# Performance work log

Measured on AMD Instinct MI355X. Metric: run time of the kernel, lower is better.

## Reference

```python
import jax, jax.numpy as jnp
import numpy as np

B, S, D = 8, 1024, 2048          # batch, seq_len, model dim (q_features == kv_features)
H, HD = 16, 128                   # num_heads, head_dim; H*HD == hidden == 2048


def setup_inputs() -> dict:
    key = jax.random.key(0)
    ks = jax.random.split(key, 6)
    fan_in = 1.0 / np.sqrt(D)     # variance_scaling(1.0, 'fan_in') style init scale
    return {
        "inputs_q": jax.random.normal(ks[0], (B, S, D), jnp.float32),
        "inputs_kv": jax.random.normal(ks[1], (B, S, D), jnp.float32),
        "Wq": jax.random.normal(ks[2], (D, H * HD), jnp.float32) * fan_in,
        "Wk": jax.random.normal(ks[3], (D, H * HD), jnp.float32) * fan_in,
        "Wv": jax.random.normal(ks[4], (D, H * HD), jnp.float32) * fan_in,
        "Wo": jax.random.normal(ks[5], (H * HD, D), jnp.float32) * (1.0 / np.sqrt(H * HD)),
    }


def reference(inputs_q, inputs_kv, Wq, Wk, Wv, Wo):
    b, sq, _ = inputs_q.shape
    skv = inputs_kv.shape[1]
    # QKV projections (DenseGeneral, no bias), reshape to heads
    # scale_attn_logits=True -> query scaled by 1/sqrt(head_dim)
    q = (inputs_q @ Wq).reshape(b, sq, H, HD) * (1.0 / np.sqrt(HD))
    k = (inputs_kv @ Wk).reshape(b, skv, H, HD)
    v = (inputs_kv @ Wv).reshape(b, skv, H, HD)
    # dot-product attention core: [b, h, q, k] scores -> softmax -> context
    scores = jnp.einsum('bqhd,bkhd->bhqk', q, k)
    attn = jax.nn.softmax(scores, axis=-1)
    ctx = jnp.einsum('bhqk,bkhd->bqhd', attn, v).reshape(b, sq, H * HD)
    # output projection back to q_features
    return ctx @ Wo
```

## Files before the change

kernel.cpp:

```cpp
#include <hip/hip_runtime.h>
#include <cstdint>
#include <cstddef>

#define B_  8
#define S_  1024
#define D_  2048
#define H_  16
#define HD_ 128

typedef __bf16 bf16x8 __attribute__((ext_vector_type(8)));
typedef float  f32x4  __attribute__((ext_vector_type(4)));

__device__ __forceinline__ unsigned short f2b(float f) {
    unsigned int u = __float_as_uint(f);
    unsigned int r = (u + 0x7fffu + ((u >> 16) & 1u)) >> 16;
    return (unsigned short)r;
}

__device__ __forceinline__ void gl2lds16(const void* g, void* l) {
    __builtin_amdgcn_global_load_lds(
        (const __attribute__((address_space(1))) void*)g,
        (__attribute__((address_space(3))) void*)l, 16, 0, 0);
}

__global__ void cvt_f32_bf16(const float* __restrict__ src,
                             unsigned short* __restrict__ dst, int n4) {
    int i = blockIdx.x * blockDim.x + threadIdx.x;
    if (i >= n4) return;
    float4 v = ((const float4*)src)[i];
    ushort4 o;
    o.x = f2b(v.x); o.y = f2b(v.y); o.z = f2b(v.z); o.w = f2b(v.w);
    ((ushort4*)dst)[i] = o;
}

__global__ void wtrans(const float* __restrict__ W, unsigned short* __restrict__ Wt) {
    __shared__ float tile[32][33];
    int bx = blockIdx.x, by = blockIdx.y;
    int tx = threadIdx.x, ty = threadIdx.y;
#pragma unroll
    for (int i = 0; i < 4; i++)
        tile[ty + i * 8][tx] = W[(size_t)(by * 32 + ty + i * 8) * D_ + bx * 32 + tx];
    __syncthreads();
#pragma unroll
    for (int i = 0; i < 4; i++)
        Wt[(size_t)(bx * 32 + ty + i * 8) * D_ + by * 32 + tx] = f2b(tile[tx][ty + i * 8]);
}

__global__ void vtrans(const unsigned short* __restrict__ V, unsigned short* __restrict__ Vt) {
    __shared__ unsigned short tile[32][33];
    int bh = blockIdx.z;
    int b = bh >> 4, h = bh & 15;
    int tx = threadIdx.x, ty = threadIdx.y;
    int s0 = blockIdx.x * 32, hd0 = blockIdx.y * 32;
#pragma unroll
    for (int i = 0; i < 4; i++)
        tile[ty + i * 8][tx] = V[(size_t)(b * S_ + s0 + ty + i * 8) * D_ + h * HD_ + hd0 + tx];
    __syncthreads();
#pragma unroll
    for (int i = 0; i < 4; i++)
        Vt[((size_t)bh * HD_ + hd0 + ty + i * 8) * S_ + s0 + tx] = tile[tx][ty + i * 8];
}

template <bool OUTF>
__global__ void gemm_bt(const unsigned short* __restrict__ A,
                        const unsigned short* __restrict__ Bt,
                        unsigned short* __restrict__ outB,
                        float* __restrict__ outF,
                        int M, int N, int K, float scale) {
    __shared__ unsigned short sA[128 * 64];
    __shared__ unsigned short sB[128 * 64];
    const int tid = threadIdx.x;
    const int w = tid >> 6, lane = tid & 63;
    const int l15 = lane & 15, lhi = lane >> 4;
    const int mBase = blockIdx.y * 128, nBase = blockIdx.x * 128;
    const int wm = (w >> 1) * 64, wn = (w & 1) * 64;

    int xoff[2];
#pragma unroll
    for (int ks = 0; ks < 2; ks++)
        xoff[ks] = (((ks * 4 + lhi) ^ (l15 & 7)) * 8);

    f32x4 acc[4][4] = {};

    for (int kb = 0; kb < K; kb += 64) {
        __syncthreads();
#pragma unroll
        for (int p = 0; p < 4; p++) {
            int c = p * 256 + tid;
            int row = c >> 3, pc = c & 7;
            int j = pc ^ (row & 7);
            gl2lds16(A  + (size_t)(mBase + row) * K + kb + j * 8, sA + c * 8);
            gl2lds16(Bt + (size_t)(nBase + row) * K + kb + j * 8, sB + c * 8);
        }
        __syncthreads();

#pragma unroll
        for (int ks = 0; ks < 2; ks++) {
            bf16x8 aF[4], bF[4];
#pragma unroll
            for (int i = 0; i < 4; i++)
                aF[i] = *(const bf16x8*)(sA + (wm + i * 16 + l15) * 64 + xoff[ks]);
#pragma unroll
            for (int j = 0; j < 4; j++)
                bF[j] = *(const bf16x8*)(sB + (wn + j * 16 + l15) * 64 + xoff[ks]);
#pragma unroll
            for (int i = 0; i < 4; i++)
#pragma unroll
                for (int j = 0; j < 4; j++)
                    acc[i][j] = __builtin_amdgcn_mfma_f32_16x16x32_bf16(aF[i], bF[j], acc[i][j], 0, 0, 0);
        }
    }

#pragma unroll
    for (int i = 0; i < 4; i++) {
#pragma unroll
        for (int j = 0; j < 4; j++) {
#pragma unroll
            for (int r = 0; r < 4; r++) {
                int row = mBase + wm + i * 16 + lhi * 4 + r;
                int col = nBase + wn + j * 16 + l15;
                float v = acc[i][j][r] * scale;
                if (OUTF) outF[(size_t)row * N + col] = v;
                else      outB[(size_t)row * N + col] = f2b(v);
            }
        }
    }
}

#define PSTR 72
__global__ void __launch_bounds__(256, 2)
attn(const unsigned short* __restrict__ Q,
     const unsigned short* __restrict__ Kb,
     const unsigned short* __restrict__ Vt,
     unsigned short* __restrict__ ctx) {
    __shared__ unsigned short sK[64 * 128];
    __shared__ unsigned short sV[128 * 64];
    __shared__ unsigned short sP[4 * 32 * PSTR];
    const int tid = threadIdx.x;
    const int w = tid >> 6, lane = tid & 63;
    const int l15 = lane & 15, lhi = lane >> 4;
    const int qt = blockIdx.x, h = blockIdx.y, b = blockIdx.z;
    const unsigned short* Qp = Q  + (size_t)b * S_ * D_ + h * HD_;
    const unsigned short* Kp = Kb + (size_t)b * S_ * D_ + h * HD_;
    const unsigned short* Vp = Vt + (size_t)(b * H_ + h) * HD_ * S_;
    const int q0 = qt * 128 + w * 32;

    int xoff[2];
#pragma unroll
    for (int ks = 0; ks < 2; ks++)
        xoff[ks] = (((ks * 4 + lhi) ^ (l15 & 7)) * 8);

    bf16x8 qF[2][4];
#pragma unroll
    for (int i = 0; i < 2; i++)
#pragma unroll
        for (int kk = 0; kk < 4; kk++)
            qF[i][kk] = *(const bf16x8*)(Qp + (size_t)(q0 + i * 16 + l15) * D_ + kk * 32 + lhi * 8);

    f32x4 o4[2][8] = {};
    float lrun[2][4] = {};
    unsigned short* sPw = sP + w * 32 * PSTR;

    for (int kt = 0; kt < S_ / 64; kt++) {
        __syncthreads();
#pragma unroll
        for (int p = 0; p < 4; p++) {
            int c = p * 256 + tid;
            {
                int row = c >> 4, pc = c & 15;
                int j = pc ^ (row & 7);
                gl2lds16(Kp + (size_t)(kt * 64 + row) * D_ + j * 8, sK + c * 8);
            }
            {
                int row = c >> 3, pc = c & 7;
                int j = pc ^ (row & 7);
                gl2lds16(Vp + (size_t)row * S_ + kt * 64 + j * 8, sV + c * 8);
            }
        }
        __syncthreads();

        f32x4 s4[2][4] = {};
#pragma unroll
        for (int j = 0; j < 4; j++) {
#pragma unroll
            for (int kk = 0; kk < 4; kk++) {
                bf16x8 bF = *(const bf16x8*)(sK + (j * 16 + l15) * 128 + ((kk * 4 + lhi) ^ (l15 & 7)) * 8);
#pragma unroll
                for (int i = 0; i < 2; i++)
                    s4[i][j] = __builtin_amdgcn_mfma_f32_16x16x32_bf16(qF[i][kk], bF, s4[i][j], 0, 0, 0);
            }
        }

#pragma unroll
        for (int i = 0; i < 2; i++) {
#pragma unroll
            for (int r = 0; r < 4; r++) {
                int prow = i * 16 + lhi * 4 + r;
                float ps = 0.f;
#pragma unroll
                for (int j = 0; j < 4; j++) {
                    float pv = exp2f(s4[i][j][r]);
                    ps += pv;
                    sPw[prow * PSTR + j * 16 + l15] = f2b(pv);
                }
                lrun[i][r] += ps;
            }
        }

#pragma unroll
        for (int k2 = 0; k2 < 2; k2++) {
            bf16x8 pF[2];
#pragma unroll
            for (int i = 0; i < 2; i++)
                pF[i] = *(const bf16x8*)(sPw + (i * 16 + l15) * PSTR + k2 * 32 + lhi * 8);
#pragma unroll
            for (int nt = 0; nt < 8; nt++) {
                bf16x8 vF = *(const bf16x8*)(sV + (nt * 16 + l15) * 64 + xoff[k2]);
#pragma unroll
                for (int i = 0; i < 2; i++)
                    o4[i][nt] = __builtin_amdgcn_mfma_f32_16x16x32_bf16(pF[i], vF, o4[i][nt], 0, 0, 0);
            }
        }
    }

#pragma unroll
    for (int i = 0; i < 2; i++)
#pragma unroll
        for (int r = 0; r < 4; r++) {
            float s = lrun[i][r];
#pragma unroll
            for (int msk = 1; msk < 16; msk <<= 1) s += __shfl_xor(s, msk);
            lrun[i][r] = 1.0f / s;
        }
#pragma unroll
    for (int i = 0; i < 2; i++)
#pragma unroll
        for (int nt = 0; nt < 8; nt++)
#pragma unroll
            for (int r = 0; r < 4; r++) {
                size_t row = (size_t)b * S_ + q0 + i * 16 + lhi * 4 + r;
                ctx[row * D_ + h * HD_ + nt * 16 + l15] = f2b(o4[i][nt][r] * lrun[i][r]);
            }
}

extern "C" void kernel_launch(void* const* d_in, const int* in_sizes, int n_in,
                              void* d_out, int out_size, void* d_ws, size_t ws_size,
                              hipStream_t stream) {
    const float* Xq  = (const float*)d_in[0];
    const float* Xkv = (const float*)d_in[1];
    const float* Wq  = (const float*)d_in[2];
    const float* Wk  = (const float*)d_in[3];
    const float* Wv  = (const float*)d_in[4];
    const float* Wo  = (const float*)d_in[5];
    float* out = (float*)d_out;

    char* ws = (char*)d_ws;
    const size_t XSZ = (size_t)B_ * S_ * D_ * 2;
    const size_t WSZ = (size_t)D_ * D_ * 2;
    unsigned short* XqB  = (unsigned short*)(ws);
    unsigned short* XkvB = (unsigned short*)(ws + XSZ);
    unsigned short* WqT  = (unsigned short*)(ws + 2 * XSZ);
    unsigned short* WkT  = (unsigned short*)(ws + 2 * XSZ + WSZ);
    unsigned short* WvT  = (unsigned short*)(ws + 2 * XSZ + 2 * WSZ);
    unsigned short* WoT  = (unsigned short*)(ws + 2 * XSZ + 3 * WSZ);
    unsigned short* Qb   = (unsigned short*)(ws + 3 * XSZ);
    unsigned short* Kb   = (unsigned short*)(ws + 4 * XSZ);
    unsigned short* Vb   = (unsigned short*)(ws + 5 * XSZ);
    unsigned short* VtB  = XkvB;
    unsigned short* ctxB = XqB;

    const int n4 = B_ * S_ * D_ / 4;
    cvt_f32_bf16<<<n4 / 256, 256, 0, stream>>>(Xq,  XqB,  n4);
    cvt_f32_bf16<<<n4 / 256, 256, 0, stream>>>(Xkv, XkvB, n4);

    dim3 tb(32, 8);
    wtrans<<<dim3(64, 64), tb, 0, stream>>>(Wq, WqT);
    wtrans<<<dim3(64, 64), tb, 0, stream>>>(Wk, WkT);
    wtrans<<<dim3(64, 64), tb, 0, stream>>>(Wv, WvT);
    wtrans<<<dim3(64, 64), tb, 0, stream>>>(Wo, WoT);

    const float qscale = 1.44269504088896f / 11.313708498984761f;
    dim3 gg(D_ / 128, B_ * S_ / 128);
    gemm_bt<false><<<gg, 256, 0, stream>>>(XqB,  WqT, Qb, nullptr, B_ * S_, D_, D_, qscale);
    gemm_bt<false><<<gg, 256, 0, stream>>>(XkvB, WkT, Kb, nullptr, B_ * S_, D_, D_, 1.0f);
    gemm_bt<false><<<gg, 256, 0, stream>>>(XkvB, WvT, Vb, nullptr, B_ * S_, D_, D_, 1.0f);

    vtrans<<<dim3(S_ / 32, HD_ / 32, B_ * H_), tb, 0, stream>>>(Vb, VtB);

    attn<<<dim3(S_ / 128, H_, B_), 256, 0, stream>>>(Qb, Kb, VtB, ctxB);

    gemm_bt<true><<<gg, 256, 0, stream>>>(ctxB, WoT, nullptr, out, B_ * S_, D_, D_, 1.0f);
}
```

Baseline: 629.7 us.

## Batch QKV projections into one launch and enlarge GEMM tile to 256x128

Replaces the generic 128x128 GEMM with a 256x128 tile kernel in which each wave computes 128x64 outputs, reusing each B fragment across eight A fragments. The three Q/K/V projections are merged into a single grid, with blockIdx.x choosing the region and its pointers, so three launches become one and the grid is larger and fuller. The output projection uses the same kernel. In exchange it needs more accumulator registers per thread (launch bounds 256,2) and more LDS per block, which may limit occupancy.

```diff
diff --git a/kernel.cpp b/kernel.cpp
--- a/kernel.cpp
+++ b/kernel.cpp
@@ -62,57 +62,71 @@
 }
 
 template <bool OUTF>
-__global__ void gemm_bt(const unsigned short* __restrict__ A,
-                        const unsigned short* __restrict__ Bt,
-                        unsigned short* __restrict__ outB,
-                        float* __restrict__ outF,
-                        int M, int N, int K, float scale) {
-    __shared__ unsigned short sA[128 * 64];
+__global__ void __launch_bounds__(256, 2)
+gemm_bt2(const unsigned short* __restrict__ A0, const unsigned short* __restrict__ A1,
+         const unsigned short* __restrict__ A2,
+         const unsigned short* __restrict__ B0, const unsigned short* __restrict__ B1,
+         const unsigned short* __restrict__ B2,
+         unsigned short* __restrict__ o0, unsigned short* __restrict__ o1,
+         unsigned short* __restrict__ o2, float* __restrict__ oF,
+         float s0, float s1, float s2) {
+    __shared__ unsigned short sA[256 * 64];
     __shared__ unsigned short sB[128 * 64];
     const int tid = threadIdx.x;
     const int w = tid >> 6, lane = tid & 63;
     const int l15 = lane & 15, lhi = lane >> 4;
-    const int mBase = blockIdx.y * 128, nBase = blockIdx.x * 128;
-    const int wm = (w >> 1) * 64, wn = (w & 1) * 64;
+    const int region = blockIdx.x >> 4;
+    const unsigned short* A  = region == 0 ? A0 : (region == 1 ? A1 : A2);
+    const unsigned short* Bt = region == 0 ? B0 : (region == 1 ? B1 : B2);
+    unsigned short* outB     = region == 0 ? o0 : (region == 1 ? o1 : o2);
+    const float scale        = region == 0 ? s0 : (region == 1 ? s1 : s2);
+    const int mBase = blockIdx.y * 256;
+    const int nBase = (blockIdx.x & 15) * 128;
+    const int wm = (w >> 1) * 128, wn = (w & 1) * 64;
 
     int xoff[2];
 #pragma unroll
     for (int ks = 0; ks < 2; ks++)
         xoff[ks] = (((ks * 4 + lhi) ^ (l15 & 7)) * 8);
 
-    f32x4 acc[4][4] = {};
-
-    for (int kb = 0; kb < K; kb += 64) {
+    f32x4 acc[8][4] = {};
+
+    for (int kb = 0; kb < D_; kb += 64) {
         __syncthreads();
+#pragma unroll
+        for (int p = 0; p < 8; p++) {
+            int c = p * 256 + tid;
+            int row = c >> 3, pc = c & 7;
+            int j = pc ^ (row & 7);
+            gl2lds16(A + (size_t)(mBase + row) * D_ + kb + j * 8, sA + c * 8);
+        }
 #pragma unroll
         for (int p = 0; p < 4; p++) {
             int c = p * 256 + tid;
             int row = c >> 3, pc = c & 7;
             int j = pc ^ (row & 7);
-            gl2lds16(A  + (size_t)(mBase + row) * K + kb + j * 8, sA + c * 8);
-            gl2lds16(Bt + (size_t)(nBase + row) * K + kb + j * 8, sB + c * 8);
+            gl2lds16(Bt + (size_t)(nBase + row) * D_ + kb + j * 8, sB + c * 8);
         }
         __syncthreads();
 
 #pragma unroll
         for (int ks = 0; ks < 2; ks++) {
-            bf16x8 aF[4], bF[4];
-#pragma unroll
-            for (int i = 0; i < 4; i++)
-                aF[i] = *(const bf16x8*)(sA + (wm + i * 16 + l15) * 64 + xoff[ks]);
+            bf16x8 bF[4];
 #pragma unroll
             for (int j = 0; j < 4; j++)
                 bF[j] = *(const bf16x8*)(sB + (wn + j * 16 + l15) * 64 + xoff[ks]);
 #pragma unroll
-            for (int i = 0; i < 4; i++)
+            for (int i = 0; i < 8; i++) {
+                bf16x8 aF = *(const bf16x8*)(sA + (wm + i * 16 + l15) * 64 + xoff[ks]);
 #pragma unroll
                 for (int j = 0; j < 4; j++)
-                    acc[i][j] = __builtin_amdgcn_mfma_f32_16x16x32_bf16(aF[i], bF[j], acc[i][j], 0, 0, 0);
+                    acc[i][j] = __builtin_amdgcn_mfma_f32_16x16x32_bf16(aF, bF[j], acc[i][j], 0, 0, 0);
+            }
         }
     }
 
 #pragma unroll
-    for (int i = 0; i < 4; i++) {
+    for (int i = 0; i < 8; i++) {
 #pragma unroll
         for (int j = 0; j < 4; j++) {
 #pragma unroll
@@ -120,8 +134,8 @@
                 int row = mBase + wm + i * 16 + lhi * 4 + r;
                 int col = nBase + wn + j * 16 + l15;
                 float v = acc[i][j][r] * scale;
-                if (OUTF) outF[(size_t)row * N + col] = v;
-                else      outB[(size_t)row * N + col] = f2b(v);
+                if (OUTF) oF[(size_t)row * D_ + col] = v;
+                else      outB[(size_t)row * D_ + col] = f2b(v);
             }
         }
     }
@@ -280,14 +294,14 @@
     wtrans<<<dim3(64, 64), tb, 0, stream>>>(Wo, WoT);
 
     const float qscale = 1.44269504088896f / 11.313708498984761f;
-    dim3 gg(D_ / 128, B_ * S_ / 128);
-    gemm_bt<false><<<gg, 256, 0, stream>>>(XqB,  WqT, Qb, nullptr, B_ * S_, D_, D_, qscale);
-    gemm_bt<false><<<gg, 256, 0, stream>>>(XkvB, WkT, Kb, nullptr, B_ * S_, D_, D_, 1.0f);
-    gemm_bt<false><<<gg, 256, 0, stream>>>(XkvB, WvT, Vb, nullptr, B_ * S_, D_, D_, 1.0f);
+
+    gemm_bt2<false><<<dim3(48, 32), 256, 0, stream>>>(
+        XqB, XkvB, XkvB, WqT, WkT, WvT, Qb, Kb, Vb, nullptr, qscale, 1.0f, 1.0f);
 
     vtrans<<<dim3(S_ / 32, HD_ / 32, B_ * H_), tb, 0, stream>>>(Vb, VtB);
 
     attn<<<dim3(S_ / 128, H_, B_), 256, 0, stream>>>(Qb, Kb, VtB, ctxB);
 
-    gemm_bt<true><<<gg, 256, 0, stream>>>(ctxB, WoT, nullptr, out, B_ * S_, D_, D_, 1.0f);
-}
+    gemm_bt2<true><<<dim3(16, 32), 256, 0, stream>>>(
+        ctxB, ctxB, ctxB, WoT, WoT, WoT, nullptr, nullptr, nullptr, out, 1.0f, 1.0f, 1.0f);
+}
```

Measured after the change: 612.8 us. -2.7%, faster.
